# Kernel optimization log

Hardware: AMD Instinct MI355X
Metric: run time of the kernel (lower is better)

## Reference

```python
import jax, jax.numpy as jnp
import numpy as np

N_NODES = 4096   # nodes in propagation tree
WORDS = 64       # word indices per node (bag-of-words)
HID = 256        # hidden_dim
VOCAB = 50257    # word_dim
NCLASS = 4
N_LEAF = 2048


def setup_inputs() -> dict:
    key = jax.random.key(0)
    ks = jax.random.split(key, 16)
    s = jnp.float32(0.1)  # init_matrix scale
    tree = jax.random.randint(ks[0], (N_NODES, WORDS), 0, VOCAB, dtype=jnp.int32)
    # parent[i] < i so node_h[parent] is already computed (topological order)
    parent = jax.random.randint(ks[1], (N_NODES,), 0, N_NODES, dtype=jnp.int32)
    parent = jnp.minimum(parent, jnp.maximum(jnp.arange(N_NODES, dtype=jnp.int32) - 1, 0))
    edge = jnp.stack([parent, jnp.arange(N_NODES, dtype=jnp.int32)], axis=1)
    leaf_idxs = jax.random.randint(ks[2], (N_LEAF,), 0, N_NODES, dtype=jnp.int32)
    y = jax.random.uniform(ks[3], (NCLASS,), dtype=jnp.float32)
    E = jax.random.normal(ks[4], (HID, VOCAB), dtype=jnp.float32) * s
    W_z = jax.random.normal(ks[5], (HID, HID), dtype=jnp.float32) * s
    U_z = jax.random.normal(ks[6], (HID, HID), dtype=jnp.float32) * s
    W_r = jax.random.normal(ks[7], (HID, HID), dtype=jnp.float32) * s
    U_r = jax.random.normal(ks[8], (HID, HID), dtype=jnp.float32) * s
    W_h = jax.random.normal(ks[9], (HID, HID), dtype=jnp.float32) * s
    U_h = jax.random.normal(ks[10], (HID, HID), dtype=jnp.float32) * s
    W_out = jax.random.normal(ks[11], (NCLASS, HID), dtype=jnp.float32) * s
    b_z = jnp.zeros((HID,), jnp.float32)
    b_r = jnp.zeros((HID,), jnp.float32)
    b_h = jnp.zeros((HID,), jnp.float32)
    b_out = jnp.zeros((NCLASS,), jnp.float32)
    return dict(tree=tree, edge=edge, leaf_idxs=leaf_idxs, y=y, E=E,
                W_z=W_z, U_z=U_z, b_z=b_z, W_r=W_r, U_r=U_r, b_r=b_r,
                W_h=W_h, U_h=U_h, b_h=b_h, W_out=W_out, b_out=b_out)


def reference(tree, edge, leaf_idxs, y, E, W_z, U_z, b_z, W_r, U_r, b_r,
              W_h, U_h, b_h, W_out, b_out):
    n_nodes = tree.shape[0]
    # child_xe per node: sum of word embeddings -> [N, HID]
    X = jnp.take(E, tree, axis=1).sum(axis=-1).T
    # W.mul(x).sum(dim=1) == W @ x; precompute input-side matvecs for all nodes
    WzX = X @ W_z.T
    WrX = X @ W_r.T
    WhX = X @ W_h.T
    node_h0 = jnp.zeros((n_nodes, X.shape[1]), X.dtype).at[0].set(X[0])

    def step(node_h, inp):
        i, wzx, wrx, whx, p = inp
        ph = node_h[p]  # parent hidden state
        z = jax.nn.sigmoid(wzx + U_z @ ph + b_z)
        r = jax.nn.sigmoid(wrx + U_r @ ph + b_r)
        c = jnp.tanh(whx + U_h @ (ph * r) + b_h)
        h = z * ph + (1.0 - z) * c
        return node_h.at[i].set(h), None

    xs = (jnp.arange(1, n_nodes), WzX[1:], WrX[1:], WhX[1:], edge[1:, 0])
    node_h, _ = jax.lax.scan(step, node_h0, xs)
    final_state = node_h[leaf_idxs].max(axis=0)  # [HID]
    pred = jax.nn.softmax(W_out @ final_state + b_out)
    loss = jnp.sum((y - pred) ** 2)
    return pred, loss
```

## Files before the change

kernel.cpp:

```cpp
#include <hip/hip_runtime.h>
#include <math.h>

#define N_NODES 4096
#define WORDS   64
#define HID     256
#define VOCAB   50257
#define NCLASS  4
#define N_LEAF  2048
#define RNN_BLOCKS 256
#define POISON 0x7FFF7FFFu

typedef _Float16 half2_t __attribute__((ext_vector_type(2)));

__device__ __forceinline__ float dot2f(half2_t a, half2_t b, float c) {
#if __has_builtin(__builtin_amdgcn_fdot2)
  return __builtin_amdgcn_fdot2(a, b, c, false);
#else
  return c + (float)a.x * (float)b.x + (float)a.y * (float)b.y;
#endif
}

__device__ __forceinline__ half2_t f2h2(float f) {
  union { float f; half2_t h; } u; u.f = f; return u.h;
}

__device__ __forceinline__ float fast_rcp(float x) { return __builtin_amdgcn_rcpf(x); }
__device__ __forceinline__ float fast_sigmoid(float x) {
  return fast_rcp(1.f + __expf(-x));
}
__device__ __forceinline__ float fast_tanh(float x) {
  return 1.f - 2.f * fast_rcp(1.f + __expf(2.f * x));
}
__device__ __forceinline__ half2_t pkrtz(float a, float b) {
#if __has_builtin(__builtin_amdgcn_cvt_pkrtz)
  return __builtin_bit_cast(half2_t, __builtin_amdgcn_cvt_pkrtz(a, b));
#else
  half2_t v; v.x = (_Float16)a; v.y = (_Float16)b; return v;
#endif
}

__global__ void poison_hpk_kernel(unsigned* __restrict__ HpkU) {
  int i = blockIdx.x * blockDim.x + threadIdx.x;
  if (i < N_NODES * (HID / 2)) HpkU[i] = POISON;
}

__global__ void transpose_f16_kernel(const float* __restrict__ src, _Float16* __restrict__ dst,
                                     int R, int C) {
  __shared__ float tile[32][33];
  int c0 = blockIdx.x * 32, r0 = blockIdx.y * 32;
  int tx = threadIdx.x, ty = threadIdx.y;
#pragma unroll
  for (int j = 0; j < 32; j += 8) {
    int c = c0 + tx, r = r0 + ty + j;
    if (c < C) tile[ty + j][tx] = src[(size_t)r * C + c];
  }
  __syncthreads();
#pragma unroll
  for (int j = 0; j < 32; j += 8) {
    int c = c0 + ty + j, r = r0 + tx;
    if (c < C) dst[(size_t)c * R + r] = (_Float16)tile[tx][ty + j];
  }
}

__global__ void __launch_bounds__(256) pack_u_kernel(
    const float* __restrict__ Uz, const float* __restrict__ Ur, const float* __restrict__ Uh,
    const float* __restrict__ Wz, const float* __restrict__ Wr, const float* __restrict__ Wh,
    half2_t* __restrict__ Upk) {
  __shared__ float tile[64][259];
  int m = blockIdx.x >> 2, g = blockIdx.x & 3;
  const float* U = m == 0 ? Uz : (m == 1 ? Ur : (m == 2 ? Uh : (m == 3 ? Wz : (m == 4 ? Wr : Wh))));
  int t = threadIdx.x;
  for (int r = 0; r < 64; ++r) tile[r][t] = U[(size_t)(g * 64 + r) * 256 + t];
  __syncthreads();
#pragma unroll
  for (int it = 0; it < 32; ++it) {
    int e = it * 256 + t;
    int hl = e & 63, kj = e >> 6, s = kj >> 5, j = kj & 31;
    half2_t v;
    v.x = (_Float16)tile[hl][s * 64 + 2 * j];
    v.y = (_Float16)tile[hl][s * 64 + 2 * j + 1];
    Upk[(size_t)(m * 4 + s) * 8192 + j * 256 + (g * 64 + hl)] = v;
  }
}

__global__ void __launch_bounds__(256) gather_gemv_kernel(
    const int* __restrict__ tree, const half2_t* __restrict__ ETh2,
    const half2_t* __restrict__ Upk,
    float* __restrict__ Az, float* __restrict__ Ar, float* __restrict__ Ah,
    float* __restrict__ H, half2_t* __restrict__ Hpk) {
  const int t  = threadIdx.x;
  const int i0 = blockIdx.x * 4;
  __shared__ int     vsf[4 * WORDS];
  __shared__ float2  ps[256];
  __shared__ half2_t Xh[4][HID / 2];

  vsf[t] = tree[(size_t)i0 * WORDS + t];
  __syncthreads();

  const int c    = t & 127;
  const int half = t >> 7;
#pragma unroll
  for (int n = 0; n < 4; ++n) {
    float ax = 0.f, ay = 0.f;
    const int base = n * WORDS + half * 32;
#pragma unroll 8
    for (int w = 0; w < 32; ++w) {
      half2_t e = ETh2[(size_t)vsf[base + w] * (HID / 2) + c];
      ax += (float)e.x;
      ay += (float)e.y;
    }
    ps[t].x = ax; ps[t].y = ay;
    __syncthreads();
    if (t < 128) {
      float xx = ps[t].x + ps[t + 128].x;
      float yy = ps[t].y + ps[t + 128].y;
      half2_t hv; hv.x = (_Float16)xx; hv.y = (_Float16)yy;
      Xh[n][t] = hv;
      if (i0 + n == 0) {
        float2 v2; v2.x = xx; v2.y = yy;
        ((float2*)H)[t] = v2;
        Hpk[t] = hv;
      }
    }
    __syncthreads();
  }

  float acc[3][4];
#pragma unroll
  for (int m = 0; m < 3; ++m)
#pragma unroll
    for (int n = 0; n < 4; ++n) acc[m][n] = 0.f;

  const half2_t* wb = Upk + (size_t)12 * 8192 + t;
#pragma unroll 8
  for (int kp = 0; kp < 128; ++kp) {
    half2_t w0 = wb[kp * 256];
    half2_t w1 = wb[kp * 256 + 32768];
    half2_t w2 = wb[kp * 256 + 65536];
    half2_t x0 = Xh[0][kp], x1 = Xh[1][kp], x2 = Xh[2][kp], x3 = Xh[3][kp];
    acc[0][0] = dot2f(w0, x0, acc[0][0]); acc[0][1] = dot2f(w0, x1, acc[0][1]);
    acc[0][2] = dot2f(w0, x2, acc[0][2]); acc[0][3] = dot2f(w0, x3, acc[0][3]);
    acc[1][0] = dot2f(w1, x0, acc[1][0]); acc[1][1] = dot2f(w1, x1, acc[1][1]);
    acc[1][2] = dot2f(w1, x2, acc[1][2]); acc[1][3] = dot2f(w1, x3, acc[1][3]);
    acc[2][0] = dot2f(w2, x0, acc[2][0]); acc[2][1] = dot2f(w2, x1, acc[2][1]);
    acc[2][2] = dot2f(w2, x2, acc[2][2]); acc[2][3] = dot2f(w2, x3, acc[2][3]);
  }
#pragma unroll
  for (int n = 0; n < 4; ++n) {
    Az[(size_t)(i0 + n) * HID + t] = acc[0][n];
    Ar[(size_t)(i0 + n) * HID + t] = acc[1][n];
    Ah[(size_t)(i0 + n) * HID + t] = acc[2][n];
  }
}

__global__ void
__attribute__((amdgpu_flat_work_group_size(512, 512), amdgpu_waves_per_eu(2, 2)))
rnn_kernel(
    const float* __restrict__ Az, const float* __restrict__ Ar, const float* __restrict__ Ah,
    const half2_t* __restrict__ Upk,
    const float* __restrict__ bz, const float* __restrict__ br, const float* __restrict__ bh,
    const int* __restrict__ edge, float* __restrict__ H, unsigned* HpkU) {
  const int tid = threadIdx.x;
  const int h   = tid & (HID - 1);
  const int ks  = tid >> 8;
  __shared__ half2_t php[HID / 2];
  __shared__ half2_t rhp[HID / 2];
  __shared__ float   part[2 * HID];

  half2_t um[128];
  half2_t uhh[64];
  {
    const half2_t* mb = Upk + (size_t)(ks ? 4 : 0) * 8192 + h;
#pragma unroll
    for (int j = 0; j < 128; ++j)
      um[j] = mb[(j >> 5) * 8192 + (j & 31) * 256];
    const half2_t* hb = Upk + (size_t)(8 + 2 * ks) * 8192 + h;
#pragma unroll
    for (int j = 0; j < 64; ++j)
      uhh[j] = hb[(j >> 5) * 8192 + (j & 31) * 256];
  }
  const float b1  = ks ? br[h] : bz[h];
  const float bhv = ks ? 0.f : bh[h];

  const int istart = blockIdx.x == 0 ? RNN_BLOCKS : blockIdx.x;
  for (int i = istart; i < N_NODES; i += RNN_BLOCKS) {
    const int p = edge[2 * i];
    const float a1 = ks ? Ar[(size_t)i * HID + h] : Az[(size_t)i * HID + h];
    const float a2 = ks ? 0.f : Ah[(size_t)i * HID + h];

    if (tid < HID / 2) {
      unsigned v = __hip_atomic_load(&HpkU[(size_t)p * (HID / 2) + tid],
                                     __ATOMIC_RELAXED, __HIP_MEMORY_SCOPE_AGENT);
      long spin = 0;
      while (v == POISON) {
        if (++spin > (1L << 22)) break;
        v = __hip_atomic_load(&HpkU[(size_t)p * (HID / 2) + tid],
                              __ATOMIC_RELAXED, __HIP_MEMORY_SCOPE_AGENT);
      }
      php[tid] = __builtin_bit_cast(half2_t, v);
    }
    __syncthreads();

    half2_t ph2 = php[h >> 1];
    const float phv = (float)((h & 1) ? ph2.y : ph2.x);

    float ac0 = a1 + b1, ac1 = 0.f, ac2 = 0.f, ac3 = 0.f;
    {
      const float4* phq = (const float4*)php;
#pragma unroll
      for (int q = 0; q < 32; ++q) {
        float4 blk = phq[q];
        ac0 = dot2f(um[4 * q + 0], f2h2(blk.x), ac0);
        ac1 = dot2f(um[4 * q + 1], f2h2(blk.y), ac1);
        ac2 = dot2f(um[4 * q + 2], f2h2(blk.z), ac2);
        ac3 = dot2f(um[4 * q + 3], f2h2(blk.w), ac3);
      }
    }
    const float g = fast_sigmoid((ac0 + ac1) + (ac2 + ac3));
    if (ks) {
      float rh = g * phv;
      float nb = __shfl_xor(rh, 1, 64);
      if ((h & 1) == 0) rhp[h >> 1] = pkrtz(rh, nb);
    }
    __syncthreads();

    float c0 = 0.f, c1 = 0.f;
    {
      const float4* rq = (const float4*)(rhp + ks * 64);
#pragma unroll
      for (int q = 0; q < 16; ++q) {
        float4 blk = rq[q];
        c0 = dot2f(uhh[4 * q + 0], f2h2(blk.x), c0);
        c1 = dot2f(uhh[4 * q + 1], f2h2(blk.y), c1);
        c0 = dot2f(uhh[4 * q + 2], f2h2(blk.z), c0);
        c1 = dot2f(uhh[4 * q + 3], f2h2(blk.w), c1);
      }
    }
    part[ks * HID + h] = c0 + c1;
    __syncthreads();

    if (ks == 0) {
      float ca = a2 + bhv + part[h] + part[HID + h];
      float c  = fast_tanh(ca);
      float hn = fmaf(g, phv, (1.f - g) * c);
      float nb = __shfl_xor(hn, 1, 64);
      if ((h & 1) == 0) {
        __hip_atomic_store(&HpkU[(size_t)i * (HID / 2) + (h >> 1)],
                           __builtin_bit_cast(unsigned, pkrtz(hn, nb)),
                           __ATOMIC_RELAXED, __HIP_MEMORY_SCOPE_AGENT);
      }
      H[(size_t)i * HID + h] = hn;
    }
  }
}

__global__ void leafmax_kernel(const float* __restrict__ H, const int* __restrict__ leafs,
                               float* __restrict__ partial) {
  int b = blockIdx.x;
  int h = threadIdx.x;
  float m = -INFINITY;
#pragma unroll 4
  for (int j = 0; j < N_LEAF / 64; ++j) {
    int node = leafs[b * (N_LEAF / 64) + j];
    m = fmaxf(m, H[(size_t)node * HID + h]);
  }
  partial[b * HID + h] = m;
}

__global__ void final_kernel(const float* __restrict__ partial, const float* __restrict__ W_out,
                             const float* __restrict__ b_out, const float* __restrict__ y,
                             float* __restrict__ out) {
  int h = threadIdx.x;
  float m = -INFINITY;
#pragma unroll 8
  for (int b = 0; b < 64; ++b) m = fmaxf(m, partial[b * HID + h]);
  __shared__ float fs[HID];
  __shared__ float red[HID];
  __shared__ float logit[NCLASS];
  fs[h] = m;
  __syncthreads();
  for (int c = 0; c < NCLASS; ++c) {
    red[h] = W_out[c * HID + h] * fs[h];
    __syncthreads();
    for (int s = HID / 2; s > 0; s >>= 1) {
      if (h < s) red[h] += red[h + s];
      __syncthreads();
    }
    if (h == 0) logit[c] = red[0] + b_out[c];
    __syncthreads();
  }
  if (h == 0) {
    float mx = logit[0];
    for (int c = 1; c < NCLASS; ++c) mx = fmaxf(mx, logit[c]);
    float e[NCLASS], s = 0.f;
    for (int c = 0; c < NCLASS; ++c) { e[c] = expf(logit[c] - mx); s += e[c]; }
    float loss = 0.f;
    for (int c = 0; c < NCLASS; ++c) {
      float p = e[c] / s;
      out[c] = p;
      float d = y[c] - p;
      loss += d * d;
    }
    out[NCLASS] = loss;
  }
}

extern "C" void kernel_launch(void* const* d_in, const int* in_sizes, int n_in,
                              void* d_out, int out_size, void* d_ws, size_t ws_size,
                              hipStream_t stream) {
  const int*   tree = (const int*)d_in[0];
  const int*   edge = (const int*)d_in[1];
  const int*   leaf = (const int*)d_in[2];
  const float* y    = (const float*)d_in[3];
  const float* E    = (const float*)d_in[4];
  const float* Wz   = (const float*)d_in[5];
  const float* Uz   = (const float*)d_in[6];
  const float* bz   = (const float*)d_in[7];
  const float* Wr   = (const float*)d_in[8];
  const float* Ur   = (const float*)d_in[9];
  const float* br   = (const float*)d_in[10];
  const float* Wh   = (const float*)d_in[11];
  const float* Uh   = (const float*)d_in[12];
  const float* bh   = (const float*)d_in[13];
  const float* Wout = (const float*)d_in[14];
  const float* bout = (const float*)d_in[15];
  float* out = (float*)d_out;

  char* base = (char*)d_ws;
  size_t b = 0;
  _Float16* ETh = (_Float16*)(base + b); b += (size_t)VOCAB * HID * 2;
  b = (b + 255) & ~(size_t)255;
  half2_t* Upk = (half2_t*)(base + b); b += (size_t)6 * 4 * 8192 * 4;
  half2_t* Hpk = (half2_t*)(base + b); b += (size_t)N_NODES * (HID / 2) * 4;
  float* Az  = (float*)(base + b); b += (size_t)N_NODES * HID * 4;
  float* Ar  = (float*)(base + b); b += (size_t)N_NODES * HID * 4;
  float* Ah  = (float*)(base + b); b += (size_t)N_NODES * HID * 4;
  float* H   = (float*)(base + b); b += (size_t)N_NODES * HID * 4;
  float* partial = (float*)(base + b); b += (size_t)64 * HID * 4;

  poison_hpk_kernel<<<(N_NODES * (HID / 2) + 255) / 256, 256, 0, stream>>>((unsigned*)Hpk);
  transpose_f16_kernel<<<dim3((VOCAB + 31) / 32, HID / 32), dim3(32, 8), 0, stream>>>(E, ETh, HID, VOCAB);
  pack_u_kernel<<<24, 256, 0, stream>>>(Uz, Ur, Uh, Wz, Wr, Wh, Upk);
  gather_gemv_kernel<<<N_NODES / 4, 256, 0, stream>>>(tree, (const half2_t*)ETh, Upk,
                                                      Az, Ar, Ah, H, Hpk);
  rnn_kernel<<<RNN_BLOCKS, 512, 0, stream>>>(Az, Ar, Ah, Upk, bz, br, bh, edge, H, (unsigned*)Hpk);
  leafmax_kernel<<<64, HID, 0, stream>>>(H, leaf, partial);
  final_kernel<<<1, HID, 0, stream>>>(partial, Wout, bout, y, out);
}
```

Baseline: 516.2 us.

## Specialize RNN block into z/r/h thread roles and prefetch next parent state

The recurrent kernel grows from 512 to 768 threads split into three roles: one each for the z gate, the r gate and the candidate. Each role holds a full 256-wide weight slice in registers, which removes the split-K partial-sum buffer and one barrier per step. While the candidate role finishes node i, the gate roles load the next node's input projections and spin-wait on its parent hidden state, overlapping that latency with the current step. In exchange, the candidate matvec is no longer split across threads, so its serial dot chain doubles in length, and the larger block runs at a tighter waves-per-EU setting.

```diff
diff --git a/kernel.cpp b/kernel.cpp
--- a/kernel.cpp
+++ b/kernel.cpp
@@ -154,95 +154,87 @@
 }
 
 __global__ void
-__attribute__((amdgpu_flat_work_group_size(512, 512), amdgpu_waves_per_eu(2, 2)))
+__attribute__((amdgpu_flat_work_group_size(768, 768), amdgpu_waves_per_eu(3, 3)))
 rnn_kernel(
     const float* __restrict__ Az, const float* __restrict__ Ar, const float* __restrict__ Ah,
     const half2_t* __restrict__ Upk,
     const float* __restrict__ bz, const float* __restrict__ br, const float* __restrict__ bh,
     const int* __restrict__ edge, float* __restrict__ H, unsigned* HpkU) {
-  const int tid = threadIdx.x;
-  const int h   = tid & (HID - 1);
-  const int ks  = tid >> 8;
+  const int tid  = threadIdx.x;
+  const int role = tid >> 8;
+  const int h    = tid & (HID - 1);
   __shared__ half2_t php[HID / 2];
   __shared__ half2_t rhp[HID / 2];
-  __shared__ float   part[2 * HID];
-
-  half2_t um[128];
-  half2_t uhh[64];
+  __shared__ float   gv[HID];
+
+  half2_t u[128];
   {
-    const half2_t* mb = Upk + (size_t)(ks ? 4 : 0) * 8192 + h;
+    const half2_t* ub = Upk + (size_t)(role * 4) * 8192 + h;
 #pragma unroll
     for (int j = 0; j < 128; ++j)
-      um[j] = mb[(j >> 5) * 8192 + (j & 31) * 256];
-    const half2_t* hb = Upk + (size_t)(8 + 2 * ks) * 8192 + h;
-#pragma unroll
-    for (int j = 0; j < 64; ++j)
-      uhh[j] = hb[(j >> 5) * 8192 + (j & 31) * 256];
-  }
-  const float b1  = ks ? br[h] : bz[h];
-  const float bhv = ks ? 0.f : bh[h];
+      u[j] = ub[(j >> 5) * 8192 + (j & 31) * 256];
+  }
+  const float  bias = role == 0 ? bz[h] : (role == 1 ? br[h] : bh[h]);
+  const float* Aptr = role == 0 ? Az : (role == 1 ? Ar : Ah);
 
   const int istart = blockIdx.x == 0 ? RNN_BLOCKS : blockIdx.x;
+
+  float a = Aptr[(size_t)istart * HID + h];
+  if (tid < HID / 2) {
+    const int p = edge[2 * istart];
+    unsigned v = __hip_atomic_load(&HpkU[(size_t)p * (HID / 2) + tid],
+                                   __ATOMIC_RELAXED, __HIP_MEMORY_SCOPE_AGENT);
+    long spin = 0;
+    while (v == POISON) {
+      if (++spin > (1L << 22)) break;
+      v = __hip_atomic_load(&HpkU[(size_t)p * (HID / 2) + tid],
+                            __ATOMIC_RELAXED, __HIP_MEMORY_SCOPE_AGENT);
+    }
+    php[tid] = __builtin_bit_cast(half2_t, v);
+  }
+
   for (int i = istart; i < N_NODES; i += RNN_BLOCKS) {
-    const int p = edge[2 * i];
-    const float a1 = ks ? Ar[(size_t)i * HID + h] : Az[(size_t)i * HID + h];
-    const float a2 = ks ? 0.f : Ah[(size_t)i * HID + h];
-
-    if (tid < HID / 2) {
-      unsigned v = __hip_atomic_load(&HpkU[(size_t)p * (HID / 2) + tid],
-                                     __ATOMIC_RELAXED, __HIP_MEMORY_SCOPE_AGENT);
-      long spin = 0;
-      while (v == POISON) {
-        if (++spin > (1L << 22)) break;
-        v = __hip_atomic_load(&HpkU[(size_t)p * (HID / 2) + tid],
-                              __ATOMIC_RELAXED, __HIP_MEMORY_SCOPE_AGENT);
-      }
-      php[tid] = __builtin_bit_cast(half2_t, v);
-    }
-    __syncthreads();
-
+    __syncthreads();
     half2_t ph2 = php[h >> 1];
     const float phv = (float)((h & 1) ? ph2.y : ph2.x);
-
-    float ac0 = a1 + b1, ac1 = 0.f, ac2 = 0.f, ac3 = 0.f;
-    {
-      const float4* phq = (const float4*)php;
+    const int inext = i + RNN_BLOCKS;
+
+    if (role < 2) {
+      const float4* vq = (const float4*)php;
+      float ac0 = 0.f, ac1 = 0.f, ac2 = 0.f, ac3 = 0.f;
 #pragma unroll
       for (int q = 0; q < 32; ++q) {
-        float4 blk = phq[q];
-        ac0 = dot2f(um[4 * q + 0], f2h2(blk.x), ac0);
-        ac1 = dot2f(um[4 * q + 1], f2h2(blk.y), ac1);
-        ac2 = dot2f(um[4 * q + 2], f2h2(blk.z), ac2);
-        ac3 = dot2f(um[4 * q + 3], f2h2(blk.w), ac3);
-      }
-    }
-    const float g = fast_sigmoid((ac0 + ac1) + (ac2 + ac3));
-    if (ks) {
-      float rh = g * phv;
-      float nb = __shfl_xor(rh, 1, 64);
-      if ((h & 1) == 0) rhp[h >> 1] = pkrtz(rh, nb);
-    }
-    __syncthreads();
-
-    float c0 = 0.f, c1 = 0.f;
-    {
-      const float4* rq = (const float4*)(rhp + ks * 64);
-#pragma unroll
-      for (int q = 0; q < 16; ++q) {
-        float4 blk = rq[q];
-        c0 = dot2f(uhh[4 * q + 0], f2h2(blk.x), c0);
-        c1 = dot2f(uhh[4 * q + 1], f2h2(blk.y), c1);
-        c0 = dot2f(uhh[4 * q + 2], f2h2(blk.z), c0);
-        c1 = dot2f(uhh[4 * q + 3], f2h2(blk.w), c1);
-      }
-    }
-    part[ks * HID + h] = c0 + c1;
-    __syncthreads();
-
-    if (ks == 0) {
-      float ca = a2 + bhv + part[h] + part[HID + h];
-      float c  = fast_tanh(ca);
-      float hn = fmaf(g, phv, (1.f - g) * c);
+        float4 blk = vq[q];
+        ac0 = dot2f(u[4 * q + 0], f2h2(blk.x), ac0);
+        ac1 = dot2f(u[4 * q + 1], f2h2(blk.y), ac1);
+        ac2 = dot2f(u[4 * q + 2], f2h2(blk.z), ac2);
+        ac3 = dot2f(u[4 * q + 3], f2h2(blk.w), ac3);
+      }
+      const float s = fast_sigmoid(a + bias + (ac0 + ac1) + (ac2 + ac3));
+      if (role == 0) {
+        gv[h] = s;
+      } else {
+        float rh = s * phv;
+        float nb = __shfl_xor(rh, 1, 64);
+        if ((h & 1) == 0) rhp[h >> 1] = pkrtz(rh, nb);
+      }
+    }
+    __syncthreads();
+
+    if (role == 2) {
+      const float4* vq = (const float4*)rhp;
+      float c0 = 0.f, c1 = 0.f, c2 = 0.f, c3 = 0.f;
+#pragma unroll
+      for (int q = 0; q < 32; ++q) {
+        float4 blk = vq[q];
+        c0 = dot2f(u[4 * q + 0], f2h2(blk.x), c0);
+        c1 = dot2f(u[4 * q + 1], f2h2(blk.y), c1);
+        c2 = dot2f(u[4 * q + 2], f2h2(blk.z), c2);
+        c3 = dot2f(u[4 * q + 3], f2h2(blk.w), c3);
+      }
+      const float c  = fast_tanh(a + bias + (c0 + c1) + (c2 + c3));
+      const float g  = gv[h];
+      const float hn = fmaf(g, phv, (1.f - g) * c);
       float nb = __shfl_xor(hn, 1, 64);
       if ((h & 1) == 0) {
         __hip_atomic_store(&HpkU[(size_t)i * (HID / 2) + (h >> 1)],
@@ -250,6 +242,21 @@
                            __ATOMIC_RELAXED, __HIP_MEMORY_SCOPE_AGENT);
       }
       H[(size_t)i * HID + h] = hn;
+      if (inext < N_NODES) a = Aptr[(size_t)inext * HID + h];
+    } else if (inext < N_NODES) {
+      a = Aptr[(size_t)inext * HID + h];
+      if (tid < HID / 2) {
+        const int pn = edge[2 * inext];
+        unsigned v = __hip_atomic_load(&HpkU[(size_t)pn * (HID / 2) + tid],
+                                       __ATOMIC_RELAXED, __HIP_MEMORY_SCOPE_AGENT);
+        long spin = 0;
+        while (v == POISON) {
+          if (++spin > (1L << 22)) break;
+          v = __hip_atomic_load(&HpkU[(size_t)pn * (HID / 2) + tid],
+                                __ATOMIC_RELAXED, __HIP_MEMORY_SCOPE_AGENT);
+        }
+        php[tid] = __builtin_bit_cast(half2_t, v);
+      }
     }
   }
 }
@@ -343,7 +350,7 @@
   pack_u_kernel<<<24, 256, 0, stream>>>(Uz, Ur, Uh, Wz, Wr, Wh, Upk);
   gather_gemv_kernel<<<N_NODES / 4, 256, 0, stream>>>(tree, (const half2_t*)ETh, Upk,
                                                       Az, Ar, Ah, H, Hpk);
-  rnn_kernel<<<RNN_BLOCKS, 512, 0, stream>>>(Az, Ar, Ah, Upk, bz, br, bh, edge, H, (unsigned*)Hpk);
+  rnn_kernel<<<RNN_BLOCKS, 768, 0, stream>>>(Az, Ar, Ah, Upk, bz, br, bh, edge, H, (unsigned*)Hpk);
   leafmax_kernel<<<64, HID, 0, stream>>>(H, leaf, partial);
   final_kernel<<<1, HID, 0, stream>>>(partial, Wout, bout, y, out);
 }
```

Measured after the change: 563.6 us. 1.09x slower.

## Process node pairs per block and forward parent state through LDS when adjacent

Applied to the files above, without the earlier changes.

Each block now handles two consecutive nodes per iteration instead of one strided node. When node i1's parent is i0, the block passes i0's packed hidden state to the second step through shared memory, so it no longer waits on a global spin-load round trip. Both parents are prefetched in one phase when they are independent. This cuts global polling latency on the serial dependency chain, at the cost of halving the number of nodes that can be in flight across blocks at once and adding an extra barrier.

```diff
diff --git a/kernel.cpp b/kernel.cpp
--- a/kernel.cpp
+++ b/kernel.cpp
@@ -163,7 +163,8 @@
   const int tid = threadIdx.x;
   const int h   = tid & (HID - 1);
   const int ks  = tid >> 8;
-  __shared__ half2_t php[HID / 2];
+  __shared__ half2_t php0[HID / 2];
+  __shared__ half2_t php1[HID / 2];
   __shared__ half2_t rhp[HID / 2];
   __shared__ float   part[2 * HID];
 
@@ -182,74 +183,149 @@
   const float b1  = ks ? br[h] : bz[h];
   const float bhv = ks ? 0.f : bh[h];
 
-  const int istart = blockIdx.x == 0 ? RNN_BLOCKS : blockIdx.x;
-  for (int i = istart; i < N_NODES; i += RNN_BLOCKS) {
-    const int p = edge[2 * i];
-    const float a1 = ks ? Ar[(size_t)i * HID + h] : Az[(size_t)i * HID + h];
-    const float a2 = ks ? 0.f : Ah[(size_t)i * HID + h];
-
-    if (tid < HID / 2) {
-      unsigned v = __hip_atomic_load(&HpkU[(size_t)p * (HID / 2) + tid],
+  for (int base = 2 * blockIdx.x; base < N_NODES; base += 2 * RNN_BLOCKS) {
+    const int i0 = base, i1 = base + 1;
+    const bool do0   = (i0 != 0);
+    const bool fast1 = do0 && (edge[2 * i1] == i0);
+
+    const float a1_0 = ks ? Ar[(size_t)i0 * HID + h] : Az[(size_t)i0 * HID + h];
+    const float a2_0 = ks ? 0.f : Ah[(size_t)i0 * HID + h];
+    const float a1_1 = ks ? Ar[(size_t)i1 * HID + h] : Az[(size_t)i1 * HID + h];
+    const float a2_1 = ks ? 0.f : Ah[(size_t)i1 * HID + h];
+
+    if (do0 && tid < HID / 2) {
+      const int p0 = edge[2 * i0];
+      unsigned v = __hip_atomic_load(&HpkU[(size_t)p0 * (HID / 2) + tid],
                                      __ATOMIC_RELAXED, __HIP_MEMORY_SCOPE_AGENT);
       long spin = 0;
       while (v == POISON) {
         if (++spin > (1L << 22)) break;
-        v = __hip_atomic_load(&HpkU[(size_t)p * (HID / 2) + tid],
+        v = __hip_atomic_load(&HpkU[(size_t)p0 * (HID / 2) + tid],
                               __ATOMIC_RELAXED, __HIP_MEMORY_SCOPE_AGENT);
       }
-      php[tid] = __builtin_bit_cast(half2_t, v);
+      php0[tid] = __builtin_bit_cast(half2_t, v);
+    }
+    if (!fast1 && tid >= HID / 2 && tid < HID) {
+      const int tl = tid - HID / 2;
+      const int p1 = edge[2 * i1];
+      unsigned v = __hip_atomic_load(&HpkU[(size_t)p1 * (HID / 2) + tl],
+                                     __ATOMIC_RELAXED, __HIP_MEMORY_SCOPE_AGENT);
+      long spin = 0;
+      while (v == POISON) {
+        if (++spin > (1L << 22)) break;
+        v = __hip_atomic_load(&HpkU[(size_t)p1 * (HID / 2) + tl],
+                              __ATOMIC_RELAXED, __HIP_MEMORY_SCOPE_AGENT);
+      }
+      php1[tl] = __builtin_bit_cast(half2_t, v);
     }
     __syncthreads();
 
-    half2_t ph2 = php[h >> 1];
-    const float phv = (float)((h & 1) ? ph2.y : ph2.x);
-
-    float ac0 = a1 + b1, ac1 = 0.f, ac2 = 0.f, ac3 = 0.f;
+    if (do0) {
+      half2_t ph2 = php0[h >> 1];
+      const float phv = (float)((h & 1) ? ph2.y : ph2.x);
+
+      float ac0 = a1_0 + b1, ac1 = 0.f, ac2 = 0.f, ac3 = 0.f;
+      {
+        const float4* phq = (const float4*)php0;
+#pragma unroll
+        for (int q = 0; q < 32; ++q) {
+          float4 blk = phq[q];
+          ac0 = dot2f(um[4 * q + 0], f2h2(blk.x), ac0);
+          ac1 = dot2f(um[4 * q + 1], f2h2(blk.y), ac1);
+          ac2 = dot2f(um[4 * q + 2], f2h2(blk.z), ac2);
+          ac3 = dot2f(um[4 * q + 3], f2h2(blk.w), ac3);
+        }
+      }
+      const float g = fast_sigmoid((ac0 + ac1) + (ac2 + ac3));
+      if (ks) {
+        float rh = g * phv;
+        float nb = __shfl_xor(rh, 1, 64);
+        if ((h & 1) == 0) rhp[h >> 1] = pkrtz(rh, nb);
+      }
+      __syncthreads();
+
+      float c0 = 0.f, c1 = 0.f;
+      {
+        const float4* rq = (const float4*)(rhp + ks * 64);
+#pragma unroll
+        for (int q = 0; q < 16; ++q) {
+          float4 blk = rq[q];
+          c0 = dot2f(uhh[4 * q + 0], f2h2(blk.x), c0);
+          c1 = dot2f(uhh[4 * q + 1], f2h2(blk.y), c1);
+          c0 = dot2f(uhh[4 * q + 2], f2h2(blk.z), c0);
+          c1 = dot2f(uhh[4 * q + 3], f2h2(blk.w), c1);
+        }
+      }
+      part[ks * HID + h] = c0 + c1;
+      __syncthreads();
+
+      if (ks == 0) {
+        float ca = a2_0 + bhv + part[h] + part[HID + h];
+        float c  = fast_tanh(ca);
+        float hn = fmaf(g, phv, (1.f - g) * c);
+        float nb = __shfl_xor(hn, 1, 64);
+        if ((h & 1) == 0) {
+          unsigned pk = __builtin_bit_cast(unsigned, pkrtz(hn, nb));
+          __hip_atomic_store(&HpkU[(size_t)i0 * (HID / 2) + (h >> 1)], pk,
+                             __ATOMIC_RELAXED, __HIP_MEMORY_SCOPE_AGENT);
+          if (fast1) php1[h >> 1] = __builtin_bit_cast(half2_t, pk);
+        }
+        H[(size_t)i0 * HID + h] = hn;
+      }
+      __syncthreads();
+    }
+
     {
-      const float4* phq = (const float4*)php;
-#pragma unroll
-      for (int q = 0; q < 32; ++q) {
-        float4 blk = phq[q];
-        ac0 = dot2f(um[4 * q + 0], f2h2(blk.x), ac0);
-        ac1 = dot2f(um[4 * q + 1], f2h2(blk.y), ac1);
-        ac2 = dot2f(um[4 * q + 2], f2h2(blk.z), ac2);
-        ac3 = dot2f(um[4 * q + 3], f2h2(blk.w), ac3);
-      }
-    }
-    const float g = fast_sigmoid((ac0 + ac1) + (ac2 + ac3));
-    if (ks) {
-      float rh = g * phv;
-      float nb = __shfl_xor(rh, 1, 64);
-      if ((h & 1) == 0) rhp[h >> 1] = pkrtz(rh, nb);
-    }
-    __syncthreads();
-
-    float c0 = 0.f, c1 = 0.f;
-    {
-      const float4* rq = (const float4*)(rhp + ks * 64);
-#pragma unroll
-      for (int q = 0; q < 16; ++q) {
-        float4 blk = rq[q];
-        c0 = dot2f(uhh[4 * q + 0], f2h2(blk.x), c0);
-        c1 = dot2f(uhh[4 * q + 1], f2h2(blk.y), c1);
-        c0 = dot2f(uhh[4 * q + 2], f2h2(blk.z), c0);
-        c1 = dot2f(uhh[4 * q + 3], f2h2(blk.w), c1);
-      }
-    }
-    part[ks * HID + h] = c0 + c1;
-    __syncthreads();
-
-    if (ks == 0) {
-      float ca = a2 + bhv + part[h] + part[HID + h];
-      float c  = fast_tanh(ca);
-      float hn = fmaf(g, phv, (1.f - g) * c);
-      float nb = __shfl_xor(hn, 1, 64);
-      if ((h & 1) == 0) {
-        __hip_atomic_store(&HpkU[(size_t)i * (HID / 2) + (h >> 1)],
-                           __builtin_bit_cast(unsigned, pkrtz(hn, nb)),
-                           __ATOMIC_RELAXED, __HIP_MEMORY_SCOPE_AGENT);
-      }
-      H[(size_t)i * HID + h] = hn;
+      half2_t ph2 = php1[h >> 1];
+      const float phv = (float)((h & 1) ? ph2.y : ph2.x);
+
+      float ac0 = a1_1 + b1, ac1 = 0.f, ac2 = 0.f, ac3 = 0.f;
+      {
+        const float4* phq = (const float4*)php1;
+#pragma unroll
+        for (int q = 0; q < 32; ++q) {
+          float4 blk = phq[q];
+          ac0 = dot2f(um[4 * q + 0], f2h2(blk.x), ac0);
+          ac1 = dot2f(um[4 * q + 1], f2h2(blk.y), ac1);
+          ac2 = dot2f(um[4 * q + 2], f2h2(blk.z), ac2);
+          ac3 = dot2f(um[4 * q + 3], f2h2(blk.w), ac3);
+        }
+      }
+      const float g = fast_sigmoid((ac0 + ac1) + (ac2 + ac3));
+      if (ks) {
+        float rh = g * phv;
+        float nb = __shfl_xor(rh, 1, 64);
+        if ((h & 1) == 0) rhp[h >> 1] = pkrtz(rh, nb);
+      }
+      __syncthreads();
+
+      float c0 = 0.f, c1 = 0.f;
+      {
+        const float4* rq = (const float4*)(rhp + ks * 64);
+#pragma unroll
+        for (int q = 0; q < 16; ++q) {
+          float4 blk = rq[q];
+          c0 = dot2f(uhh[4 * q + 0], f2h2(blk.x), c0);
+          c1 = dot2f(uhh[4 * q + 1], f2h2(blk.y), c1);
+          c0 = dot2f(uhh[4 * q + 2], f2h2(blk.z), c0);
+          c1 = dot2f(uhh[4 * q + 3], f2h2(blk.w), c1);
+        }
+      }
+      part[ks * HID + h] = c0 + c1;
+      __syncthreads();
+
+      if (ks == 0) {
+        float ca = a2_1 + bhv + part[h] + part[HID + h];
+        float c  = fast_tanh(ca);
+        float hn = fmaf(g, phv, (1.f - g) * c);
+        float nb = __shfl_xor(hn, 1, 64);
+        if ((h & 1) == 0) {
+          __hip_atomic_store(&HpkU[(size_t)i1 * (HID / 2) + (h >> 1)],
+                             __builtin_bit_cast(unsigned, pkrtz(hn, nb)),
+                             __ATOMIC_RELAXED, __HIP_MEMORY_SCOPE_AGENT);
+        }
+        H[(size_t)i1 * HID + h] = hn;
+      }
     }
   }
 }
```

Result: slower. 619.7 us (+20.1%).

## Fuse embedding gather and input GEMV into persistent RNN kernel prologue

Applied to the files above, without the earlier changes.

Each persistent RNN block now gathers the embeddings and computes the W_z/W_r/W_h input projections in a prologue, for exactly the 16 nodes it will later process. The results stay in LDS instead of going through global Az/Ar/Ah buffers. Poisoning of the hidden-state array is folded into extra blocks of the pack kernel, which removes two kernel launches and a round trip to global memory. The cost is much more LDS per block and a serial prologue on only 256 blocks, which delays the start of the recurrent chain.

```diff
diff --git a/kernel.cpp b/kernel.cpp
--- a/kernel.cpp
+++ b/kernel.cpp
@@ -39,11 +39,6 @@
 #endif
 }
 
-__global__ void poison_hpk_kernel(unsigned* __restrict__ HpkU) {
-  int i = blockIdx.x * blockDim.x + threadIdx.x;
-  if (i < N_NODES * (HID / 2)) HpkU[i] = POISON;
-}
-
 __global__ void transpose_f16_kernel(const float* __restrict__ src, _Float16* __restrict__ dst,
                                      int R, int C) {
   __shared__ float tile[32][33];
@@ -65,7 +60,13 @@
 __global__ void __launch_bounds__(256) pack_u_kernel(
     const float* __restrict__ Uz, const float* __restrict__ Ur, const float* __restrict__ Uh,
     const float* __restrict__ Wz, const float* __restrict__ Wr, const float* __restrict__ Wh,
-    half2_t* __restrict__ Upk) {
+    half2_t* __restrict__ Upk, unsigned* __restrict__ HpkU) {
+  if (blockIdx.x >= 24) {
+    int base = (blockIdx.x - 24) * 16384 + threadIdx.x;
+#pragma unroll
+    for (int k = 0; k < 64; ++k) HpkU[base + k * 256] = POISON;
+    return;
+  }
   __shared__ float tile[64][259];
   int m = blockIdx.x >> 2, g = blockIdx.x & 3;
   const float* U = m == 0 ? Uz : (m == 1 ? Ur : (m == 2 ? Uh : (m == 3 ? Wz : (m == 4 ? Wr : Wh))));
@@ -83,89 +84,107 @@
   }
 }
 
-__global__ void __launch_bounds__(256) gather_gemv_kernel(
-    const int* __restrict__ tree, const half2_t* __restrict__ ETh2,
-    const half2_t* __restrict__ Upk,
-    float* __restrict__ Az, float* __restrict__ Ar, float* __restrict__ Ah,
-    float* __restrict__ H, half2_t* __restrict__ Hpk) {
-  const int t  = threadIdx.x;
-  const int i0 = blockIdx.x * 4;
-  __shared__ int     vsf[4 * WORDS];
-  __shared__ float2  ps[256];
-  __shared__ half2_t Xh[4][HID / 2];
-
-  vsf[t] = tree[(size_t)i0 * WORDS + t];
-  __syncthreads();
-
-  const int c    = t & 127;
-  const int half = t >> 7;
-#pragma unroll
-  for (int n = 0; n < 4; ++n) {
-    float ax = 0.f, ay = 0.f;
-    const int base = n * WORDS + half * 32;
-#pragma unroll 8
-    for (int w = 0; w < 32; ++w) {
-      half2_t e = ETh2[(size_t)vsf[base + w] * (HID / 2) + c];
-      ax += (float)e.x;
-      ay += (float)e.y;
-    }
-    ps[t].x = ax; ps[t].y = ay;
-    __syncthreads();
-    if (t < 128) {
-      float xx = ps[t].x + ps[t + 128].x;
-      float yy = ps[t].y + ps[t + 128].y;
-      half2_t hv; hv.x = (_Float16)xx; hv.y = (_Float16)yy;
-      Xh[n][t] = hv;
-      if (i0 + n == 0) {
-        float2 v2; v2.x = xx; v2.y = yy;
-        ((float2*)H)[t] = v2;
-        Hpk[t] = hv;
-      }
-    }
-    __syncthreads();
-  }
-
-  float acc[3][4];
-#pragma unroll
-  for (int m = 0; m < 3; ++m)
-#pragma unroll
-    for (int n = 0; n < 4; ++n) acc[m][n] = 0.f;
-
-  const half2_t* wb = Upk + (size_t)12 * 8192 + t;
-#pragma unroll 8
-  for (int kp = 0; kp < 128; ++kp) {
-    half2_t w0 = wb[kp * 256];
-    half2_t w1 = wb[kp * 256 + 32768];
-    half2_t w2 = wb[kp * 256 + 65536];
-    half2_t x0 = Xh[0][kp], x1 = Xh[1][kp], x2 = Xh[2][kp], x3 = Xh[3][kp];
-    acc[0][0] = dot2f(w0, x0, acc[0][0]); acc[0][1] = dot2f(w0, x1, acc[0][1]);
-    acc[0][2] = dot2f(w0, x2, acc[0][2]); acc[0][3] = dot2f(w0, x3, acc[0][3]);
-    acc[1][0] = dot2f(w1, x0, acc[1][0]); acc[1][1] = dot2f(w1, x1, acc[1][1]);
-    acc[1][2] = dot2f(w1, x2, acc[1][2]); acc[1][3] = dot2f(w1, x3, acc[1][3]);
-    acc[2][0] = dot2f(w2, x0, acc[2][0]); acc[2][1] = dot2f(w2, x1, acc[2][1]);
-    acc[2][2] = dot2f(w2, x2, acc[2][2]); acc[2][3] = dot2f(w2, x3, acc[2][3]);
-  }
-#pragma unroll
-  for (int n = 0; n < 4; ++n) {
-    Az[(size_t)(i0 + n) * HID + t] = acc[0][n];
-    Ar[(size_t)(i0 + n) * HID + t] = acc[1][n];
-    Ah[(size_t)(i0 + n) * HID + t] = acc[2][n];
-  }
-}
-
 __global__ void
 __attribute__((amdgpu_flat_work_group_size(512, 512), amdgpu_waves_per_eu(2, 2)))
 rnn_kernel(
-    const float* __restrict__ Az, const float* __restrict__ Ar, const float* __restrict__ Ah,
+    const int* __restrict__ tree, const half2_t* __restrict__ ETh2,
     const half2_t* __restrict__ Upk,
     const float* __restrict__ bz, const float* __restrict__ br, const float* __restrict__ bh,
     const int* __restrict__ edge, float* __restrict__ H, unsigned* HpkU) {
   const int tid = threadIdx.x;
   const int h   = tid & (HID - 1);
   const int ks  = tid >> 8;
+  const int b   = blockIdx.x;
   __shared__ half2_t php[HID / 2];
   __shared__ half2_t rhp[HID / 2];
   __shared__ float   part[2 * HID];
+  __shared__ int     vsAll[16][WORDS];
+  __shared__ float2  ps16[16][4][HID / 2];
+  __shared__ half2_t Xh[16][HID / 2];
+  __shared__ float   ldsA[16][3][HID];
+
+#pragma unroll
+  for (int m2 = 0; m2 < 2; ++m2) {
+    int idx = tid + m2 * 512;
+    int n = idx >> 6, w = idx & 63;
+    vsAll[n][w] = tree[(size_t)(b + (n << 8)) * WORDS + w];
+  }
+  __syncthreads();
+
+  {
+    const int c = tid & 127;
+    const int g = tid >> 7;
+    float ax[16], ay[16];
+#pragma unroll
+    for (int n = 0; n < 16; ++n) { ax[n] = 0.f; ay[n] = 0.f; }
+#pragma unroll
+    for (int n = 0; n < 16; ++n) {
+#pragma unroll
+      for (int w = 0; w < 16; ++w) {
+        half2_t e = ETh2[(size_t)vsAll[n][g * 16 + w] * (HID / 2) + c];
+        ax[n] += (float)e.x;
+        ay[n] += (float)e.y;
+      }
+    }
+#pragma unroll
+    for (int n = 0; n < 16; ++n) { ps16[n][g][c].x = ax[n]; ps16[n][g][c].y = ay[n]; }
+  }
+  __syncthreads();
+
+#pragma unroll
+  for (int k = 0; k < 4; ++k) {
+    int o = tid + k * 512;
+    int n = o >> 7, c = o & 127;
+    float xx = (ps16[n][0][c].x + ps16[n][1][c].x) + (ps16[n][2][c].x + ps16[n][3][c].x);
+    float yy = (ps16[n][0][c].y + ps16[n][1][c].y) + (ps16[n][2][c].y + ps16[n][3][c].y);
+    half2_t hv; hv.x = (_Float16)xx; hv.y = (_Float16)yy;
+    Xh[n][c] = hv;
+    if (b == 0 && n == 0) {
+      float2 v2; v2.x = xx; v2.y = yy;
+      ((float2*)H)[c] = v2;
+      __hip_atomic_store(&HpkU[c], __builtin_bit_cast(unsigned, hv),
+                         __ATOMIC_RELAXED, __HIP_MEMORY_SCOPE_AGENT);
+    }
+  }
+  __syncthreads();
+
+  {
+    float az[16], ar[16], ah[16];
+#pragma unroll
+    for (int n = 0; n < 16; ++n) { az[n] = 0.f; ar[n] = 0.f; ah[n] = 0.f; }
+    const half2_t* wb = Upk + (size_t)98304 + h;
+    const int kp0 = ks * 64;
+#pragma unroll 4
+    for (int kp = kp0; kp < kp0 + 64; ++kp) {
+      half2_t w0 = wb[kp * 256];
+      half2_t w1 = wb[kp * 256 + 32768];
+      half2_t w2 = wb[kp * 256 + 65536];
+#pragma unroll
+      for (int n = 0; n < 16; ++n) {
+        half2_t x = Xh[n][kp];
+        az[n] = dot2f(w0, x, az[n]);
+        ar[n] = dot2f(w1, x, ar[n]);
+        ah[n] = dot2f(w2, x, ah[n]);
+      }
+    }
+    if (ks == 0) {
+#pragma unroll
+      for (int n = 0; n < 16; ++n) {
+        ldsA[n][0][h] = az[n]; ldsA[n][1][h] = ar[n]; ldsA[n][2][h] = ah[n];
+      }
+    }
+    __syncthreads();
+    if (ks == 1) {
+#pragma unroll
+      for (int n = 0; n < 16; ++n) {
+        ldsA[n][0][h] += az[n]; ldsA[n][1][h] += ar[n]; ldsA[n][2][h] += ah[n];
+      }
+    }
+    __syncthreads();
+  }
+#if __has_builtin(__builtin_amdgcn_sched_barrier)
+  __builtin_amdgcn_sched_barrier(0);
+#endif
 
   half2_t um[128];
   half2_t uhh[64];
@@ -182,11 +201,12 @@
   const float b1  = ks ? br[h] : bz[h];
   const float bhv = ks ? 0.f : bh[h];
 
-  const int istart = blockIdx.x == 0 ? RNN_BLOCKS : blockIdx.x;
+  const int istart = b == 0 ? RNN_BLOCKS : b;
   for (int i = istart; i < N_NODES; i += RNN_BLOCKS) {
     const int p = edge[2 * i];
-    const float a1 = ks ? Ar[(size_t)i * HID + h] : Az[(size_t)i * HID + h];
-    const float a2 = ks ? 0.f : Ah[(size_t)i * HID + h];
+    const int r = i >> 8;
+    const float a1 = ks ? ldsA[r][1][h] : ldsA[r][0][h];
+    const float a2 = ks ? 0.f : ldsA[r][2][h];
 
     if (tid < HID / 2) {
       unsigned v = __hip_atomic_load(&HpkU[(size_t)p * (HID / 2) + tid],
@@ -332,18 +352,13 @@
   b = (b + 255) & ~(size_t)255;
   half2_t* Upk = (half2_t*)(base + b); b += (size_t)6 * 4 * 8192 * 4;
   half2_t* Hpk = (half2_t*)(base + b); b += (size_t)N_NODES * (HID / 2) * 4;
-  float* Az  = (float*)(base + b); b += (size_t)N_NODES * HID * 4;
-  float* Ar  = (float*)(base + b); b += (size_t)N_NODES * HID * 4;
-  float* Ah  = (float*)(base + b); b += (size_t)N_NODES * HID * 4;
   float* H   = (float*)(base + b); b += (size_t)N_NODES * HID * 4;
   float* partial = (float*)(base + b); b += (size_t)64 * HID * 4;
 
-  poison_hpk_kernel<<<(N_NODES * (HID / 2) + 255) / 256, 256, 0, stream>>>((unsigned*)Hpk);
   transpose_f16_kernel<<<dim3((VOCAB + 31) / 32, HID / 32), dim3(32, 8), 0, stream>>>(E, ETh, HID, VOCAB);
-  pack_u_kernel<<<24, 256, 0, stream>>>(Uz, Ur, Uh, Wz, Wr, Wh, Upk);
-  gather_gemv_kernel<<<N_NODES / 4, 256, 0, stream>>>(tree, (const half2_t*)ETh, Upk,
-                                                      Az, Ar, Ah, H, Hpk);
-  rnn_kernel<<<RNN_BLOCKS, 512, 0, stream>>>(Az, Ar, Ah, Upk, bz, br, bh, edge, H, (unsigned*)Hpk);
+  pack_u_kernel<<<56, 256, 0, stream>>>(Uz, Ur, Uh, Wz, Wr, Wh, Upk, (unsigned*)Hpk);
+  rnn_kernel<<<RNN_BLOCKS, 512, 0, stream>>>(tree, (const half2_t*)ETh, Upk,
+                                             bz, br, bh, edge, H, (unsigned*)Hpk);
   leafmax_kernel<<<64, HID, 0, stream>>>(H, leaf, partial);
   final_kernel<<<1, HID, 0, stream>>>(partial, Wout, bout, y, out);
 }
```

Result: slower. 562.8 us (+9.0%).
